# Kernel optimization log

Measured on AMD Instinct MI355X. Metric: run time of the kernel, lower is better.

## Reference

```python
import jax, jax.numpy as jnp
import numpy as np

B, T, H, N = 4, 2048, 1024, 16
DT_MIN, DT_MAX = 1e-3, 1e-1
A_INIT_MIN, A_INIT_MAX = 0.5, 2.0


def _inv_softplus(x):
    # log(exp(x) - 1), numerically stable
    return x + jnp.log(-jnp.expm1(-x))


def setup_inputs() -> dict:
    key = jax.random.key(0)
    kx, ka, kb, kc, kw, kdt = jax.random.split(key, 6)
    x = jax.random.normal(kx, (B, T, H), dtype=jnp.float32)
    A_log = jax.random.uniform(ka, (H, N), minval=np.log(A_INIT_MIN), maxval=np.log(A_INIT_MAX), dtype=jnp.float32)
    B_mat = 0.02 * jax.random.normal(kb, (H, N), dtype=jnp.float32)
    C_mat = 0.02 * jax.random.normal(kc, (H, N), dtype=jnp.float32)
    D_vec = jnp.ones((H,), dtype=jnp.float32)
    W_dt = 0.02 * jax.random.normal(kw, (H, H), dtype=jnp.float32)
    b_dt = _inv_softplus(jax.random.uniform(kdt, (H,), minval=DT_MIN, maxval=DT_MAX, dtype=jnp.float32))
    return {"x": x, "A_log": A_log, "B_mat": B_mat, "C_mat": C_mat, "D_vec": D_vec, "W_dt": W_dt, "b_dt": b_dt}


def reference(x, A_log, B_mat, C_mat, D_vec, W_dt, b_dt):
    # in_proj is Identity since input_size == hidden_size
    u = x  # (B, T, H)
    A = -jnp.exp(A_log)  # (H, N)
    # dt for all timesteps at once: softplus(u @ W_dt^T + b_dt) -> (B, T, H)
    dt = jax.nn.softplus(jnp.einsum('bth,gh->btg', u, W_dt) + b_dt)
    state0 = jnp.zeros((u.shape[0], A_log.shape[0], A_log.shape[1]), dtype=u.dtype)

    def step(state, inp):
        dt_t, u_t = inp  # (B, H), (B, H)
        dtA = dt_t[..., None]  # (B, H, 1)
        A_bar = jnp.exp(dtA * A)                       # (B, H, N)
        state = A_bar * state + (dtA * B_mat) * u_t[..., None]
        y_t = jnp.einsum('bhn,hn->bh', state, C_mat) + D_vec * u_t
        return state, y_t

    # scan over time axis
    state_final, ys = jax.lax.scan(step, state0, (dt.transpose(1, 0, 2), u.transpose(1, 0, 2)))
    out = ys.transpose(1, 0, 2)  # (B, T, H)
    return out, state_final
```

## Files before the change

### kernel.cpp

```cpp
#include <hip/hip_runtime.h>
#include <stdint.h>

#define BB 4
#define TT 2048
#define HH 1024
#define NN 16
#define KK 1024
#define GG 1024
#define MM (BB*TT)
#define NCHUNK 64
#define TC (TT/NCHUNK)
#define HB 256

#if __has_builtin(__builtin_amdgcn_exp2f)
#define FAST_EXP2(x) __builtin_amdgcn_exp2f(x)
#else
#define FAST_EXP2(x) __expf((x) * 0.6931471805599453f)
#endif
#define EXPSCALE 1.4426950408889634f

typedef __attribute__((ext_vector_type(8))) short short8;
typedef __attribute__((ext_vector_type(4))) float f32x4;

__device__ __forceinline__ unsigned short f2bf(float f) {
  union { float f; unsigned u; } a; a.f = f;
  unsigned u = a.u;
  u += 0x7fffu + ((u >> 16) & 1u);
  return (unsigned short)(u >> 16);
}

__global__ __launch_bounds__(256) void cvt2_f32_bf16(const float* __restrict__ srcA,
                                                     unsigned short* __restrict__ dstA, int n4a,
                                                     const float* __restrict__ srcB,
                                                     unsigned short* __restrict__ dstB, int n4b) {
  int i = blockIdx.x * blockDim.x + threadIdx.x;
  const float* s; unsigned short* d; int j;
  if (i < n4a) { s = srcA; d = dstA; j = i; }
  else         { s = srcB; d = dstB; j = i - n4a; if (j >= n4b) return; }
  float4 a = ((const float4*)s)[j];
  ushort4 o;
  o.x = f2bf(a.x); o.y = f2bf(a.y); o.z = f2bf(a.z); o.w = f2bf(a.w);
  ((ushort4*)d)[j] = o;
}

__global__ __launch_bounds__(256, 4) void gemm_dt(const unsigned short* __restrict__ xb,
                                                  const unsigned short* __restrict__ wb,
                                                  const float* __restrict__ b_dt,
                                                  _Float16* __restrict__ dtH) {
  __shared__ short lsA[128 * 64];
  __shared__ short lsB[64 * 64];
  const int tid  = threadIdx.x;
  const int w    = tid >> 6;
  const int lane = tid & 63;
  const int bid  = blockIdx.x;
  const int swz  = (bid & 7) * 128 + (bid >> 3);
  const int m0 = (swz >> 4) * 128;
  const int g0 = (swz & 15) * 64;

  const int r8 = lane >> 3;
  const int c8 = (lane & 7) * 8;
  const unsigned short* gA[4];
  short*                lA[4];
#pragma unroll
  for (int q = 0; q < 4; ++q) {
    const int row = w * 32 + q * 8 + r8;
    gA[q] = xb + (size_t)(m0 + row) * KK + c8;
    lA[q] = lsA + row * 64;
  }
  const unsigned short* gB[2];
  short*                lB[2];
#pragma unroll
  for (int q = 0; q < 2; ++q) {
    const int row = w * 16 + q * 8 + r8;
    gB[q] = wb + (size_t)(g0 + row) * KK + c8;
    lB[q] = lsB + row * 64;
  }

  const int wm   = (w >> 1) * 64;
  const int wg   = (w & 1) * 32;
  const int lrow = lane & 15;
  const int lq   = lane >> 4;

  int aoff[4][2], boff[2][2];
#pragma unroll
  for (int mi = 0; mi < 4; ++mi) {
    const int row = wm + mi * 16 + lrow;
    aoff[mi][0] = row * 64 + lq * 8;
    aoff[mi][1] = row * 64 + 32 + lq * 8;
  }
#pragma unroll
  for (int ni = 0; ni < 2; ++ni) {
    const int row = wg + ni * 16 + lrow;
    boff[ni][0] = row * 64 + lq * 8;
    boff[ni][1] = row * 64 + 32 + lq * 8;
  }

  f32x4 acc[4][2];
  const f32x4 zero = {0.f, 0.f, 0.f, 0.f};
#pragma unroll
  for (int i = 0; i < 4; ++i)
#pragma unroll
    for (int j = 0; j < 2; ++j) acc[i][j] = zero;

  for (int kt = 0; kt < KK / 64; ++kt) {
    const int ko = kt * 64;
#pragma unroll
    for (int q = 0; q < 4; ++q)
      __builtin_amdgcn_global_load_lds((__attribute__((address_space(1))) void*)(gA[q] + ko),
                                       (__attribute__((address_space(3))) void*)(lA[q]), 16, 0, 0);
#pragma unroll
    for (int q = 0; q < 2; ++q)
      __builtin_amdgcn_global_load_lds((__attribute__((address_space(1))) void*)(gB[q] + ko),
                                       (__attribute__((address_space(3))) void*)(lB[q]), 16, 0, 0);
    __syncthreads();

#pragma unroll
    for (int kk = 0; kk < 2; ++kk) {
      short8 af[4], bfr[2];
#pragma unroll
      for (int mi = 0; mi < 4; ++mi) af[mi] = *(const short8*)&lsA[aoff[mi][kk]];
#pragma unroll
      for (int ni = 0; ni < 2; ++ni) bfr[ni] = *(const short8*)&lsB[boff[ni][kk]];
#pragma unroll
      for (int mi = 0; mi < 4; ++mi)
#pragma unroll
        for (int ni = 0; ni < 2; ++ni)
          acc[mi][ni] = __builtin_amdgcn_mfma_f32_16x16x32_bf16(af[mi], bfr[ni], acc[mi][ni], 0, 0, 0);
    }
    __syncthreads();
  }

  const int mrow = m0 + wm + lq * 4;
#pragma unroll
  for (int ni = 0; ni < 2; ++ni) {
    const int g = g0 + wg + ni * 16 + lrow;
    const float bias = b_dt[g];
#pragma unroll
    for (int mi = 0; mi < 4; ++mi)
#pragma unroll
      for (int r = 0; r < 4; ++r) {
        float z = acc[mi][ni][r] + bias;
        dtH[(size_t)(mrow + mi * 16 + r) * GG + g] =
            (_Float16)(fmaxf(z, 0.f) + __logf(1.f + __expf(-fabsf(z))));
      }
  }
}

__global__ __launch_bounds__(256, 4) void ssm_phase1(const float* __restrict__ x,
                                                     const _Float16* __restrict__ dtH,
                                                     const float* __restrict__ A_log,
                                                     float* __restrict__ sloc,
                                                     float* __restrict__ sdArr) {
  const int tid = threadIdx.x;
  const int bid = blockIdx.x;
  const int hb = bid & (HH / HB - 1);
  const int b  = (bid >> 2) & (BB - 1);
  const int c  = bid >> 4;
  const int h  = hb * HB + tid;

  const size_t base = ((size_t)b * TT + c * TC) * HH + h;
  const float*    up = x + base;
  const _Float16* dp = dtH + base;

  float Ae[NN];
#pragma unroll
  for (int n = 0; n < NN; n += 4) {
    f32x4 av = *(const f32x4*)&A_log[h * NN + n];
#pragma unroll
    for (int q = 0; q < 4; ++q) Ae[n + q] = -__expf(av[q]) * EXPSCALE;
  }

  float s[NN];
#pragma unroll
  for (int n = 0; n < NN; ++n) s[n] = 0.f;
  float sd = 0.f;

#pragma unroll
  for (int j = 0; j < TC / 8; ++j) {
    float uu[8], dv[8];
#pragma unroll
    for (int i = 0; i < 8; ++i) {
      uu[i] = up[(size_t)(j * 8 + i) * HH];
      dv[i] = (float)dp[(size_t)(j * 8 + i) * HH];
    }
#pragma unroll
    for (int i = 0; i < 8; ++i) {
      const float dtv = dv[i];
      const float du  = dtv * uu[i];
      sd += dtv;
#pragma unroll
      for (int n = 0; n < NN; ++n) {
        const float ab = FAST_EXP2(dtv * Ae[n]);
        s[n] = fmaf(ab, s[n], du);
      }
    }
  }

  float* sp = sloc + (((size_t)c * BB + b) * HH + h) * NN;
#pragma unroll
  for (int n = 0; n < NN; n += 4) {
    f32x4 v = {s[n], s[n + 1], s[n + 2], s[n + 3]};
    *(f32x4*)&sp[n] = v;
  }
  sdArr[((size_t)c * BB + b) * HH + h] = sd;
}

__global__ __launch_bounds__(256) void ssm_phase2(float* __restrict__ sloc,
                                                  const float* __restrict__ sdArr,
                                                  const float* __restrict__ A_log,
                                                  const float* __restrict__ Bm_,
                                                  float* __restrict__ stateOut) {
  const int id = blockIdx.x * 256 + threadIdx.x;
  const int hn = id & (HH * NN - 1);
  const int bh = id >> 4;
  const float Ae = -__expf(A_log[hn]) * EXPSCALE;
  float carry = 0.f;
#pragma unroll 8
  for (int ch = 0; ch < NCHUNK; ++ch) {
    const size_t idx = (size_t)ch * (BB * HH * NN) + id;
    const float sl = sloc[idx];
    const float dc = FAST_EXP2(Ae * sdArr[(size_t)ch * (BB * HH) + bh]);
    sloc[idx] = carry;
    carry = fmaf(dc, carry, sl);
  }
  stateOut[id] = Bm_[hn] * carry;
}

__global__ __launch_bounds__(256, 4) void ssm_phase3(const float* __restrict__ x,
                                                     const _Float16* __restrict__ dtH,
                                                     const float* __restrict__ A_log,
                                                     const float* __restrict__ Bm_,
                                                     const float* __restrict__ Cm_,
                                                     const float* __restrict__ Dv_,
                                                     const float* __restrict__ carryBuf,
                                                     float* __restrict__ out) {
  const int tid = threadIdx.x;
  const int bid = blockIdx.x;
  const int hb = bid & (HH / HB - 1);
  const int b  = (bid >> 2) & (BB - 1);
  const int c  = bid >> 4;
  const int h  = hb * HB + tid;

  const size_t base = ((size_t)b * TT + c * TC) * HH + h;
  const float*    up = x + base;
  const _Float16* dp = dtH + base;
  float*          yo = out + base;

  float Ae[NN], Cb[NN];
#pragma unroll
  for (int n = 0; n < NN; n += 4) {
    f32x4 av = *(const f32x4*)&A_log[h * NN + n];
    f32x4 cv = *(const f32x4*)&Cm_[h * NN + n];
    f32x4 bv = *(const f32x4*)&Bm_[h * NN + n];
#pragma unroll
    for (int q = 0; q < 4; ++q) {
      Ae[n + q] = -__expf(av[q]) * EXPSCALE;
      Cb[n + q] = cv[q] * bv[q];
    }
  }
  const float Dv = Dv_[h];

  float s[NN];
  const float* cp = carryBuf + (((size_t)c * BB + b) * HH + h) * NN;
#pragma unroll
  for (int n = 0; n < NN; n += 4) {
    f32x4 v = *(const f32x4*)&cp[n];
    s[n] = v[0]; s[n + 1] = v[1]; s[n + 2] = v[2]; s[n + 3] = v[3];
  }

#pragma unroll
  for (int j = 0; j < TC / 8; ++j) {
    float uu[8], dv[8];
#pragma unroll
    for (int i = 0; i < 8; ++i) {
      uu[i] = up[(size_t)(j * 8 + i) * HH];
      dv[i] = (float)dp[(size_t)(j * 8 + i) * HH];
    }
#pragma unroll
    for (int i = 0; i < 8; ++i) {
      const float dtv = dv[i];
      const float uv  = uu[i];
      const float du  = dtv * uv;
      float y0 = Dv * uv, y1 = 0.f, y2 = 0.f, y3 = 0.f;
#pragma unroll
      for (int n = 0; n < NN; n += 4) {
        float ab;
        ab = FAST_EXP2(dtv * Ae[n]);     s[n]     = fmaf(ab, s[n],     du); y0 = fmaf(Cb[n],     s[n],     y0);
        ab = FAST_EXP2(dtv * Ae[n + 1]); s[n + 1] = fmaf(ab, s[n + 1], du); y1 = fmaf(Cb[n + 1], s[n + 1], y1);
        ab = FAST_EXP2(dtv * Ae[n + 2]); s[n + 2] = fmaf(ab, s[n + 2], du); y2 = fmaf(Cb[n + 2], s[n + 2], y2);
        ab = FAST_EXP2(dtv * Ae[n + 3]); s[n + 3] = fmaf(ab, s[n + 3], du); y3 = fmaf(Cb[n + 3], s[n + 3], y3);
      }
      yo[(size_t)(j * 8 + i) * HH] = (y0 + y1) + (y2 + y3);
    }
  }
}

extern "C" void kernel_launch(void* const* d_in, const int* in_sizes, int n_in,
                              void* d_out, int out_size, void* d_ws, size_t ws_size,
                              hipStream_t stream) {
  const float* x     = (const float*)d_in[0];
  const float* A_log = (const float*)d_in[1];
  const float* B_mat = (const float*)d_in[2];
  const float* C_mat = (const float*)d_in[3];
  const float* D_vec = (const float*)d_in[4];
  const float* W_dt  = (const float*)d_in[5];
  const float* b_dt  = (const float*)d_in[6];
  float* out = (float*)d_out;

  char* ws = (char*)d_ws;
  unsigned short* xb   = (unsigned short*)(ws);
  unsigned short* wb   = (unsigned short*)(ws + 16777216);
  _Float16*       dtH  = (_Float16*)(ws + 18874368);
  float*          sloc  = (float*)(ws);
  float*          sdArr = (float*)(ws + 16777216);
  float* stateOut = out + (size_t)BB * TT * HH;

  const int n4x = MM * KK / 4, n4w = GG * KK / 4;
  cvt2_f32_bf16<<<(n4x + n4w + 255) / 256, 256, 0, stream>>>(x, xb, n4x, W_dt, wb, n4w);
  gemm_dt<<<(MM / 128) * (GG / 64), 256, 0, stream>>>(xb, wb, b_dt, dtH);

  const int nblk = (HH / HB) * BB * NCHUNK;
  ssm_phase1<<<nblk, 256, 0, stream>>>(x, dtH, A_log, sloc, sdArr);
  ssm_phase2<<<(BB * HH * NN) / 256, 256, 0, stream>>>(sloc, sdArr, A_log, B_mat, stateOut);
  ssm_phase3<<<nblk, 256, 0, stream>>>(x, dtH, A_log, B_mat, C_mat, D_vec, sloc, out);
}
```

Baseline: 180.4 us.

## Read bf16 x in scan phases, double chunks, transpose chunk-state layout

The scan phases now read the bf16 copy of x made for the GEMM instead of the fp32 input, which halves that input traffic. The chunk count doubles so each chunk is shorter and there are more blocks, and occupancy hints rise to 8 blocks per CU. The per-chunk state buffers are moved into a separate workspace region and laid out n-major so stores and loads coalesce across h. This is meant to cut memory traffic and raise parallelism, but the u term in the recurrence and the D*u skip term now use bf16-rounded values, which lowers accuracy, and phase 2 does twice as many serial carry steps.

```diff
diff --git a/kernel.cpp b/kernel.cpp
--- a/kernel.cpp
+++ b/kernel.cpp
@@ -8,7 +8,7 @@
 #define KK 1024
 #define GG 1024
 #define MM (BB*TT)
-#define NCHUNK 64
+#define NCHUNK 128
 #define TC (TT/NCHUNK)
 #define HB 256
 
@@ -27,6 +27,11 @@
   unsigned u = a.u;
   u += 0x7fffu + ((u >> 16) & 1u);
   return (unsigned short)(u >> 16);
+}
+
+__device__ __forceinline__ float bf2f(unsigned short v) {
+  union { unsigned u; float f; } a; a.u = ((unsigned)v) << 16;
+  return a.f;
 }
 
 __global__ __launch_bounds__(256) void cvt2_f32_bf16(const float* __restrict__ srcA,
@@ -146,21 +151,21 @@
   }
 }
 
-__global__ __launch_bounds__(256, 4) void ssm_phase1(const float* __restrict__ x,
+__global__ __launch_bounds__(256, 8) void ssm_phase1(const unsigned short* __restrict__ xb,
                                                      const _Float16* __restrict__ dtH,
                                                      const float* __restrict__ A_log,
                                                      float* __restrict__ sloc,
                                                      float* __restrict__ sdArr) {
   const int tid = threadIdx.x;
   const int bid = blockIdx.x;
-  const int hb = bid & (HH / HB - 1);
+  const int hb = bid & 3;
   const int b  = (bid >> 2) & (BB - 1);
   const int c  = bid >> 4;
   const int h  = hb * HB + tid;
 
   const size_t base = ((size_t)b * TT + c * TC) * HH + h;
-  const float*    up = x + base;
-  const _Float16* dp = dtH + base;
+  const unsigned short* up = xb + base;
+  const _Float16*       dp = dtH + base;
 
   float Ae[NN];
 #pragma unroll
@@ -176,17 +181,17 @@
   float sd = 0.f;
 
 #pragma unroll
-  for (int j = 0; j < TC / 8; ++j) {
-    float uu[8], dv[8];
-#pragma unroll
-    for (int i = 0; i < 8; ++i) {
-      uu[i] = up[(size_t)(j * 8 + i) * HH];
-      dv[i] = (float)dp[(size_t)(j * 8 + i) * HH];
-    }
-#pragma unroll
-    for (int i = 0; i < 8; ++i) {
-      const float dtv = dv[i];
-      const float du  = dtv * uu[i];
+  for (int j = 0; j < TC / 4; ++j) {
+    unsigned short uu[4]; _Float16 dv[4];
+#pragma unroll
+    for (int i = 0; i < 4; ++i) {
+      uu[i] = up[(size_t)(j * 4 + i) * HH];
+      dv[i] = dp[(size_t)(j * 4 + i) * HH];
+    }
+#pragma unroll
+    for (int i = 0; i < 4; ++i) {
+      const float dtv = (float)dv[i];
+      const float du  = dtv * bf2f(uu[i]);
       sd += dtv;
 #pragma unroll
       for (int n = 0; n < NN; ++n) {
@@ -196,13 +201,10 @@
     }
   }
 
-  float* sp = sloc + (((size_t)c * BB + b) * HH + h) * NN;
-#pragma unroll
-  for (int n = 0; n < NN; n += 4) {
-    f32x4 v = {s[n], s[n + 1], s[n + 2], s[n + 3]};
-    *(f32x4*)&sp[n] = v;
-  }
-  sdArr[((size_t)c * BB + b) * HH + h] = sd;
+  float* sp = sloc + ((size_t)(c * BB + b) * NN) * HH + h;
+#pragma unroll
+  for (int n = 0; n < NN; ++n) sp[(size_t)n * HH] = s[n];
+  sdArr[(size_t)(c * BB + b) * HH + h] = sd;
 }
 
 __global__ __launch_bounds__(256) void ssm_phase2(float* __restrict__ sloc,
@@ -211,8 +213,11 @@
                                                   const float* __restrict__ Bm_,
                                                   float* __restrict__ stateOut) {
   const int id = blockIdx.x * 256 + threadIdx.x;
-  const int hn = id & (HH * NN - 1);
-  const int bh = id >> 4;
+  const int h  = id & (HH - 1);
+  const int n  = (id >> 10) & (NN - 1);
+  const int b  = id >> 14;
+  const int hn = h * NN + n;
+  const int bh = b * HH + h;
   const float Ae = -__expf(A_log[hn]) * EXPSCALE;
   float carry = 0.f;
 #pragma unroll 8
@@ -223,10 +228,10 @@
     sloc[idx] = carry;
     carry = fmaf(dc, carry, sl);
   }
-  stateOut[id] = Bm_[hn] * carry;
-}
-
-__global__ __launch_bounds__(256, 4) void ssm_phase3(const float* __restrict__ x,
+  stateOut[(size_t)bh * NN + n] = Bm_[hn] * carry;
+}
+
+__global__ __launch_bounds__(256, 8) void ssm_phase3(const unsigned short* __restrict__ xb,
                                                      const _Float16* __restrict__ dtH,
                                                      const float* __restrict__ A_log,
                                                      const float* __restrict__ Bm_,
@@ -236,15 +241,15 @@
                                                      float* __restrict__ out) {
   const int tid = threadIdx.x;
   const int bid = blockIdx.x;
-  const int hb = bid & (HH / HB - 1);
+  const int hb = bid & 3;
   const int b  = (bid >> 2) & (BB - 1);
   const int c  = bid >> 4;
   const int h  = hb * HB + tid;
 
   const size_t base = ((size_t)b * TT + c * TC) * HH + h;
-  const float*    up = x + base;
-  const _Float16* dp = dtH + base;
-  float*          yo = out + base;
+  const unsigned short* up = xb + base;
+  const _Float16*       dp = dtH + base;
+  float*                yo = out + base;
 
   float Ae[NN], Cb[NN];
 #pragma unroll
@@ -261,37 +266,23 @@
   const float Dv = Dv_[h];
 
   float s[NN];
-  const float* cp = carryBuf + (((size_t)c * BB + b) * HH + h) * NN;
-#pragma unroll
-  for (int n = 0; n < NN; n += 4) {
-    f32x4 v = *(const f32x4*)&cp[n];
-    s[n] = v[0]; s[n + 1] = v[1]; s[n + 2] = v[2]; s[n + 3] = v[3];
-  }
-
-#pragma unroll
-  for (int j = 0; j < TC / 8; ++j) {
-    float uu[8], dv[8];
-#pragma unroll
-    for (int i = 0; i < 8; ++i) {
-      uu[i] = up[(size_t)(j * 8 + i) * HH];
-      dv[i] = (float)dp[(size_t)(j * 8 + i) * HH];
-    }
-#pragma unroll
-    for (int i = 0; i < 8; ++i) {
-      const float dtv = dv[i];
-      const float uv  = uu[i];
-      const float du  = dtv * uv;
-      float y0 = Dv * uv, y1 = 0.f, y2 = 0.f, y3 = 0.f;
-#pragma unroll
-      for (int n = 0; n < NN; n += 4) {
-        float ab;
-        ab = FAST_EXP2(dtv * Ae[n]);     s[n]     = fmaf(ab, s[n],     du); y0 = fmaf(Cb[n],     s[n],     y0);
-        ab = FAST_EXP2(dtv * Ae[n + 1]); s[n + 1] = fmaf(ab, s[n + 1], du); y1 = fmaf(Cb[n + 1], s[n + 1], y1);
-        ab = FAST_EXP2(dtv * Ae[n + 2]); s[n + 2] = fmaf(ab, s[n + 2], du); y2 = fmaf(Cb[n + 2], s[n + 2], y2);
-        ab = FAST_EXP2(dtv * Ae[n + 3]); s[n + 3] = fmaf(ab, s[n + 3], du); y3 = fmaf(Cb[n + 3], s[n + 3], y3);
-      }
-      yo[(size_t)(j * 8 + i) * HH] = (y0 + y1) + (y2 + y3);
-    }
+  const float* cp = carryBuf + ((size_t)(c * BB + b) * NN) * HH + h;
+#pragma unroll
+  for (int n = 0; n < NN; ++n) s[n] = cp[(size_t)n * HH];
+
+#pragma unroll
+  for (int t = 0; t < TC; ++t) {
+    const float dtv = (float)dp[(size_t)t * HH];
+    const float uv  = bf2f(up[(size_t)t * HH]);
+    const float du  = dtv * uv;
+    float y0 = Dv * uv, y1 = 0.f;
+#pragma unroll
+    for (int n = 0; n < NN; n += 2) {
+      float ab;
+      ab = FAST_EXP2(dtv * Ae[n]);     s[n]     = fmaf(ab, s[n],     du); y0 = fmaf(Cb[n],     s[n],     y0);
+      ab = FAST_EXP2(dtv * Ae[n + 1]); s[n + 1] = fmaf(ab, s[n + 1], du); y1 = fmaf(Cb[n + 1], s[n + 1], y1);
+    }
+    yo[(size_t)t * HH] = y0 + y1;
   }
 }
 
@@ -308,11 +299,11 @@
   float* out = (float*)d_out;
 
   char* ws = (char*)d_ws;
-  unsigned short* xb   = (unsigned short*)(ws);
-  unsigned short* wb   = (unsigned short*)(ws + 16777216);
-  _Float16*       dtH  = (_Float16*)(ws + 18874368);
-  float*          sloc  = (float*)(ws);
-  float*          sdArr = (float*)(ws + 16777216);
+  unsigned short* xb    = (unsigned short*)(ws);
+  unsigned short* wb    = (unsigned short*)(ws + 16777216);
+  _Float16*       dtH   = (_Float16*)(ws + 18874368);
+  float*          sloc  = (float*)(ws + 35651584);
+  float*          sdArr = (float*)(ws + 69206016);
   float* stateOut = out + (size_t)BB * TT * HH;
 
   const int n4x = MM * KK / 4, n4w = GG * KK / 4;
@@ -320,7 +311,7 @@
   gemm_dt<<<(MM / 128) * (GG / 64), 256, 0, stream>>>(xb, wb, b_dt, dtH);
 
   const int nblk = (HH / HB) * BB * NCHUNK;
-  ssm_phase1<<<nblk, 256, 0, stream>>>(x, dtH, A_log, sloc, sdArr);
+  ssm_phase1<<<nblk, 256, 0, stream>>>(xb, dtH, A_log, sloc, sdArr);
   ssm_phase2<<<(BB * HH * NN) / 256, 256, 0, stream>>>(sloc, sdArr, A_log, B_mat, stateOut);
-  ssm_phase3<<<nblk, 256, 0, stream>>>(x, dtH, A_log, B_mat, C_mat, D_vec, sloc, out);
-}
+  ssm_phase3<<<nblk, 256, 0, stream>>>(xb, dtH, A_log, B_mat, C_mat, D_vec, sloc, out);
+}
```

After: 234.6 us. +30.0%, slower.
